# Optimization experiments

Measured on AMD Instinct MI355X. Metric: run time of the kernel, lower is better.

## Reference

```python
import jax, jax.numpy as jnp
import numpy as np

# BCQLinear packed forward: weight[o, i] reconstructed from per-(out,group,bit)
# alpha scales and +/-1 binary codes via einsum('oib,oiab->oia'), then a plain
# out-channel-wise matmul (in_ch_wise=False) plus bias. beta is NOT used in the
# packed forward path of the original module.

B, S = 2, 1024          # token dims (m...)
O = 4096                 # out_features
G, A, NB = 32, 128, 3    # n_groups, group_size, n_bits; in_features = G*A = 4096


def setup_inputs() -> dict:
    key = jax.random.key(0)
    k1, k2, k3, k4 = jax.random.split(key, 4)
    x = jax.random.normal(k1, (B, S, G * A), dtype=jnp.float32)
    # binary codes are strictly +/-1 (Packer.unpack yields sign bits)
    b = jnp.sign(jax.random.normal(k2, (O, G, A, NB)))
    binary = jnp.where(b == 0, 1.0, b).astype(jnp.float32)
    # alpha scales are small positive magnitudes in practice
    alpha = jax.random.uniform(k3, (O, G, NB), dtype=jnp.float32,
                               minval=0.01, maxval=0.1)
    bias = 0.01 * jax.random.normal(k4, (O,), dtype=jnp.float32)
    return {"input": x, "binary": binary, "alpha": alpha, "bias": bias}


def reference(input, binary, alpha, bias):
    # dequantize: [O, G, A] -> [O, I]
    weight = jnp.einsum('oib,oiab->oia', alpha, binary).reshape(binary.shape[0], -1)
    # out-channel-wise matmul: m...i, oi -> m...o
    out = jnp.einsum('msi,oi->mso', input, weight) + bias
    return out
```

## Files before the change

### kernel.cpp

```cpp
#include <hip/hip_runtime.h>
#include <hip/hip_bf16.h>
#include <stdint.h>

typedef __bf16 bf16x8 __attribute__((ext_vector_type(8)));
typedef __bf16 bf16x4 __attribute__((ext_vector_type(4)));
typedef float  f32x4  __attribute__((ext_vector_type(4)));

static constexpr int Mdim = 2048;
static constexpr int Ndim = 4096;
static constexpr int Kdim = 4096;
static constexpr int DQ_BLOCKS = (Ndim * Kdim / 4) / 256;
static constexpr int CVT_BLOCKS = (Mdim * Kdim / 8) / 256;

__global__ __launch_bounds__(256)
void prep(const float* __restrict__ binary, const float* __restrict__ alpha,
          const float* __restrict__ x, __bf16* __restrict__ w,
          __bf16* __restrict__ xb) {
  const int b = blockIdx.x;
  if (b < DQ_BLOCKS) {
    long e = ((long)b * 256 + threadIdx.x) * 4;
    int o = (int)(e >> 12);
    int i = (int)(e & 4095);
    int g = i >> 7;
    const float* al = alpha + ((long)o * 32 + g) * 3;
    float a0 = al[0], a1 = al[1], a2 = al[2];
    const float4* bs = (const float4*)(binary + e * 3);
    float4 b0 = bs[0], b1 = bs[1], b2 = bs[2];
    bf16x4 wv;
    wv[0] = (__bf16)(a0 * b0.x + a1 * b0.y + a2 * b0.z);
    wv[1] = (__bf16)(a0 * b0.w + a1 * b1.x + a2 * b1.y);
    wv[2] = (__bf16)(a0 * b1.z + a1 * b1.w + a2 * b2.x);
    wv[3] = (__bf16)(a0 * b2.y + a1 * b2.z + a2 * b2.w);
    *(bf16x4*)(w + e) = wv;
  } else {
    long e = ((long)(b - DQ_BLOCKS) * 256 + threadIdx.x) * 8;
    float4 v0 = *(const float4*)(x + e);
    float4 v1 = *(const float4*)(x + e + 4);
    bf16x8 r;
    r[0] = (__bf16)v0.x; r[1] = (__bf16)v0.y; r[2] = (__bf16)v0.z; r[3] = (__bf16)v0.w;
    r[4] = (__bf16)v1.x; r[5] = (__bf16)v1.y; r[6] = (__bf16)v1.z; r[7] = (__bf16)v1.w;
    *(bf16x8*)(xb + e) = r;
  }
}

static constexpr int NT = Kdim / 64;
static constexpr int BUF = 49152;

__device__ __forceinline__ void g2l16(const void* g, void* l) {
  __builtin_amdgcn_global_load_lds(
      (const __attribute__((address_space(1))) void*)g,
      (__attribute__((address_space(3))) void*)l, 16, 0, 0);
}

#define BAR()    __builtin_amdgcn_s_barrier()
#define LGKM0()  asm volatile("s_waitcnt lgkmcnt(0)" ::: "memory")
#define SCHED0() __builtin_amdgcn_sched_barrier(0)
#define VMC6()   asm volatile("s_waitcnt vmcnt(6)" ::: "memory")
#define VMC0()   asm volatile("s_waitcnt vmcnt(0)" ::: "memory")

#define STAGE_A(t, H, bo) do { \
  _Pragma("unroll") for (int j_ = 0; j_ < 2; ++j_) \
    g2l16(baseA[j_] + (H) * 128 * (long)Kdim + (t) * 64, \
          sm + (bo) + (H) * 16384 + (w * 2 + j_) * 1024); \
} while (0)
#define STAGE_B(t, bo) do { \
  _Pragma("unroll") for (int j_ = 0; j_ < 2; ++j_) \
    g2l16(baseB[j_] + (t) * 64, \
          sm + (bo) + 32768 + (w * 2 + j_) * 1024); \
} while (0)

#define LOAD_A4(dst, bo, m0_) do { \
  _Pragma("unroll") for (int m_ = 0; m_ < 4; ++m_) \
    _Pragma("unroll") for (int h_ = 0; h_ < 2; ++h_) \
      dst[m_][h_] = *(const bf16x8*)(sm + (bo) + aoffbase + ((m0_) + m_) * 2048 + swz[h_]); \
} while (0)
#define LOAD_B2(dst, bo) do { \
  _Pragma("unroll") for (int n_ = 0; n_ < 2; ++n_) \
    _Pragma("unroll") for (int h_ = 0; h_ < 2; ++h_) \
      dst[n_][h_] = *(const bf16x8*)(sm + (bo) + boffbase + n_ * 2048 + swz[h_]); \
} while (0)

#define MMA16(fa_, fb_, m0_) do { \
  __builtin_amdgcn_s_setprio(1); \
  _Pragma("unroll") for (int m_ = 0; m_ < 4; ++m_) \
    _Pragma("unroll") for (int n_ = 0; n_ < 2; ++n_) { \
      acc[(m0_) + m_][n_] = __builtin_amdgcn_mfma_f32_16x16x32_bf16( \
          fa_[m_][0], fb_[n_][0], acc[(m0_) + m_][n_], 0, 0, 0); \
      acc[(m0_) + m_][n_] = __builtin_amdgcn_mfma_f32_16x16x32_bf16( \
          fa_[m_][1], fb_[n_][1], acc[(m0_) + m_][n_], 0, 0, 0); \
    } \
  __builtin_amdgcn_s_setprio(0); \
} while (0)

__global__ __launch_bounds__(512, 2)
void gemm3(const __bf16* __restrict__ A, const __bf16* __restrict__ Bw,
           const float* __restrict__ bias, float* __restrict__ out) {
  __shared__ __align__(128) char sm[3 * BUF];
  const int tid = threadIdx.x, lane = tid & 63, w = tid >> 6;
  const int wm = w >> 2, wn = w & 3;

  const int bid = blockIdx.x;
  const int logical = (bid & 7) * 32 + (bid >> 3);
  const int tm = logical & 7;
  const int tn = logical >> 3;

  const int rlo = lane >> 3;
  const int gsw = (lane & 7) ^ rlo;
  const __bf16* baseA[2];
  const __bf16* baseB[2];
#pragma unroll
  for (int j = 0; j < 2; ++j) {
    int rp = (w * 2 + j) * 8 + rlo;
    baseA[j] = A  + (long)(tm * 256 + rp) * Kdim + gsw * 8;
    baseB[j] = Bw + (long)(tn * 128 + rp) * Kdim + gsw * 8;
  }

  int swz[2];
#pragma unroll
  for (int h = 0; h < 2; ++h)
    swz[h] = (((h * 4 + (lane >> 4)) ^ (lane & 7)) << 4);
  const int aoffbase = (wm * 128 + (lane & 15)) * 128;
  const int boffbase = 32768 + (wn * 32 + (lane & 15)) * 128;

  f32x4 acc[8][2] = {};

  STAGE_A(0, 0, 0);     STAGE_A(0, 1, 0);     STAGE_B(0, 0);
  STAGE_A(1, 0, BUF);   STAGE_A(1, 1, BUF);   STAGE_B(1, BUF);
  VMC6();
  BAR();

  bf16x8 fa[4][2], fa2[4][2], fb[2][2];
  int ba = 0, bb = BUF, bc = 2 * BUF;

  for (int t = 0; t < NT; ++t) {
    const bool pf = (t + 2 < NT);
    LOAD_A4(fa, ba, 0);
    LOAD_B2(fb, ba);
    if (pf) STAGE_A(t + 2, 0, bc);
    BAR(); LGKM0(); SCHED0();
    MMA16(fa, fb, 0);
    BAR();
    LOAD_A4(fa2, ba, 4);
    if (pf) { STAGE_A(t + 2, 1, bc); STAGE_B(t + 2, bc); }
    if (t < NT - 2) { VMC6(); } else { VMC0(); }
    BAR(); LGKM0(); SCHED0();
    MMA16(fa2, fb, 4);
    BAR();
    int tmp = ba; ba = bb; bb = bc; bc = tmp;
  }

  const int r4 = (lane >> 4) * 4;
  const int cl = lane & 15;
#pragma unroll
  for (int n = 0; n < 2; ++n) {
    const int col = tn * 128 + wn * 32 + n * 16 + cl;
    const float bv = bias[col];
#pragma unroll
    for (int m = 0; m < 8; ++m)
#pragma unroll
      for (int r = 0; r < 4; ++r) {
        const int row = tm * 256 + wm * 128 + m * 16 + r4 + r;
        out[(long)row * Ndim + col] = acc[m][n][r] + bv;
      }
  }
}

extern "C" void kernel_launch(void* const* d_in, const int* in_sizes, int n_in,
                              void* d_out, int out_size, void* d_ws, size_t ws_size,
                              hipStream_t stream) {
  const float* x      = (const float*)d_in[0];
  const float* binary = (const float*)d_in[1];
  const float* alpha  = (const float*)d_in[2];
  const float* bias   = (const float*)d_in[3];
  float* out = (float*)d_out;

  __bf16* wb = (__bf16*)d_ws;
  __bf16* xb = wb + (size_t)Ndim * Kdim;

  prep<<<dim3(DQ_BLOCKS + CVT_BLOCKS), 256, 0, stream>>>(binary, alpha, x, wb, xb);
  gemm3<<<dim3(256), 512, 0, stream>>>(xb, wb, bias, out);
}
```

Measured before the change: 122.8 us.

## Transpose GEMM tile to 128x256, stage epilogue through LDS, widen dequant

```diff
diff --git a/kernel.cpp b/kernel.cpp
--- a/kernel.cpp
+++ b/kernel.cpp
@@ -3,13 +3,12 @@
 #include <stdint.h>
 
 typedef __bf16 bf16x8 __attribute__((ext_vector_type(8)));
-typedef __bf16 bf16x4 __attribute__((ext_vector_type(4)));
 typedef float  f32x4  __attribute__((ext_vector_type(4)));
 
 static constexpr int Mdim = 2048;
 static constexpr int Ndim = 4096;
 static constexpr int Kdim = 4096;
-static constexpr int DQ_BLOCKS = (Ndim * Kdim / 4) / 256;
+static constexpr int DQ_BLOCKS = (Ndim * Kdim / 8) / 256;
 static constexpr int CVT_BLOCKS = (Mdim * Kdim / 8) / 256;
 
 __global__ __launch_bounds__(256)
@@ -18,20 +17,23 @@
           __bf16* __restrict__ xb) {
   const int b = blockIdx.x;
   if (b < DQ_BLOCKS) {
-    long e = ((long)b * 256 + threadIdx.x) * 4;
+    long e = ((long)b * 256 + threadIdx.x) * 8;
     int o = (int)(e >> 12);
-    int i = (int)(e & 4095);
-    int g = i >> 7;
+    int g = (int)((e & 4095) >> 7);
     const float* al = alpha + ((long)o * 32 + g) * 3;
     float a0 = al[0], a1 = al[1], a2 = al[2];
-    const float4* bs = (const float4*)(binary + e * 3);
-    float4 b0 = bs[0], b1 = bs[1], b2 = bs[2];
-    bf16x4 wv;
-    wv[0] = (__bf16)(a0 * b0.x + a1 * b0.y + a2 * b0.z);
-    wv[1] = (__bf16)(a0 * b0.w + a1 * b1.x + a2 * b1.y);
-    wv[2] = (__bf16)(a0 * b1.z + a1 * b1.w + a2 * b2.x);
-    wv[3] = (__bf16)(a0 * b2.y + a1 * b2.z + a2 * b2.w);
-    *(bf16x4*)(w + e) = wv;
+    const float4* q = (const float4*)(binary + e * 3);
+    float4 q0 = q[0], q1 = q[1], q2 = q[2], q3 = q[3], q4 = q[4], q5 = q[5];
+    bf16x8 wv;
+    wv[0] = (__bf16)(a0 * q0.x + a1 * q0.y + a2 * q0.z);
+    wv[1] = (__bf16)(a0 * q0.w + a1 * q1.x + a2 * q1.y);
+    wv[2] = (__bf16)(a0 * q1.z + a1 * q1.w + a2 * q2.x);
+    wv[3] = (__bf16)(a0 * q2.y + a1 * q2.z + a2 * q2.w);
+    wv[4] = (__bf16)(a0 * q3.x + a1 * q3.y + a2 * q3.z);
+    wv[5] = (__bf16)(a0 * q3.w + a1 * q4.x + a2 * q4.y);
+    wv[6] = (__bf16)(a0 * q4.z + a1 * q4.w + a2 * q5.x);
+    wv[7] = (__bf16)(a0 * q5.y + a1 * q5.z + a2 * q5.w);
+    *(bf16x8*)(w + e) = wv;
   } else {
     long e = ((long)(b - DQ_BLOCKS) * 256 + threadIdx.x) * 8;
     float4 v0 = *(const float4*)(x + e);
@@ -58,42 +60,40 @@
 #define VMC6()   asm volatile("s_waitcnt vmcnt(6)" ::: "memory")
 #define VMC0()   asm volatile("s_waitcnt vmcnt(0)" ::: "memory")
 
-#define STAGE_A(t, H, bo) do { \
+#define STAGE_A(t, bo) do { \
   _Pragma("unroll") for (int j_ = 0; j_ < 2; ++j_) \
-    g2l16(baseA[j_] + (H) * 128 * (long)Kdim + (t) * 64, \
-          sm + (bo) + (H) * 16384 + (w * 2 + j_) * 1024); \
+    g2l16(baseA[j_] + (t) * 64, sm + (bo) + (w * 2 + j_) * 1024); \
 } while (0)
 #define STAGE_B(t, bo) do { \
-  _Pragma("unroll") for (int j_ = 0; j_ < 2; ++j_) \
-    g2l16(baseB[j_] + (t) * 64, \
-          sm + (bo) + 32768 + (w * 2 + j_) * 1024); \
+  _Pragma("unroll") for (int j_ = 0; j_ < 4; ++j_) \
+    g2l16(baseB[j_] + (t) * 64, sm + (bo) + 16384 + (w * 4 + j_) * 1024); \
 } while (0)
 
-#define LOAD_A4(dst, bo, m0_) do { \
+#define LOAD_A4(dst, bo) do { \
   _Pragma("unroll") for (int m_ = 0; m_ < 4; ++m_) \
     _Pragma("unroll") for (int h_ = 0; h_ < 2; ++h_) \
-      dst[m_][h_] = *(const bf16x8*)(sm + (bo) + aoffbase + ((m0_) + m_) * 2048 + swz[h_]); \
+      dst[m_][h_] = *(const bf16x8*)(sm + (bo) + aoffbase + m_ * 2048 + swz[h_]); \
 } while (0)
-#define LOAD_B2(dst, bo) do { \
+#define LOAD_B2(dst, bo, n0_) do { \
   _Pragma("unroll") for (int n_ = 0; n_ < 2; ++n_) \
     _Pragma("unroll") for (int h_ = 0; h_ < 2; ++h_) \
-      dst[n_][h_] = *(const bf16x8*)(sm + (bo) + boffbase + n_ * 2048 + swz[h_]); \
+      dst[n_][h_] = *(const bf16x8*)(sm + (bo) + boffbase + ((n0_) + n_) * 2048 + swz[h_]); \
 } while (0)
 
-#define MMA16(fa_, fb_, m0_) do { \
+#define MMA16(fa_, fb_, n0_) do { \
   __builtin_amdgcn_s_setprio(1); \
   _Pragma("unroll") for (int m_ = 0; m_ < 4; ++m_) \
     _Pragma("unroll") for (int n_ = 0; n_ < 2; ++n_) { \
-      acc[(m0_) + m_][n_] = __builtin_amdgcn_mfma_f32_16x16x32_bf16( \
-          fa_[m_][0], fb_[n_][0], acc[(m0_) + m_][n_], 0, 0, 0); \
-      acc[(m0_) + m_][n_] = __builtin_amdgcn_mfma_f32_16x16x32_bf16( \
-          fa_[m_][1], fb_[n_][1], acc[(m0_) + m_][n_], 0, 0, 0); \
+      acc[m_][(n0_) + n_] = __builtin_amdgcn_mfma_f32_16x16x32_bf16( \
+          fa_[m_][0], fb_[n_][0], acc[m_][(n0_) + n_], 0, 0, 0); \
+      acc[m_][(n0_) + n_] = __builtin_amdgcn_mfma_f32_16x16x32_bf16( \
+          fa_[m_][1], fb_[n_][1], acc[m_][(n0_) + n_], 0, 0, 0); \
     } \
   __builtin_amdgcn_s_setprio(0); \
 } while (0)
 
 __global__ __launch_bounds__(512, 2)
-void gemm3(const __bf16* __restrict__ A, const __bf16* __restrict__ Bw,
+void gemm4(const __bf16* __restrict__ A, const __bf16* __restrict__ Bw,
            const float* __restrict__ bias, float* __restrict__ out) {
   __shared__ __align__(128) char sm[3 * BUF];
   const int tid = threadIdx.x, lane = tid & 63, w = tid >> 6;
@@ -101,67 +101,77 @@
 
   const int bid = blockIdx.x;
   const int logical = (bid & 7) * 32 + (bid >> 3);
-  const int tm = logical & 7;
-  const int tn = logical >> 3;
+  const int tm = logical & 15;
+  const int tn = logical >> 4;
 
   const int rlo = lane >> 3;
   const int gsw = (lane & 7) ^ rlo;
   const __bf16* baseA[2];
-  const __bf16* baseB[2];
+  const __bf16* baseB[4];
 #pragma unroll
-  for (int j = 0; j < 2; ++j) {
-    int rp = (w * 2 + j) * 8 + rlo;
-    baseA[j] = A  + (long)(tm * 256 + rp) * Kdim + gsw * 8;
-    baseB[j] = Bw + (long)(tn * 128 + rp) * Kdim + gsw * 8;
-  }
+  for (int j = 0; j < 2; ++j)
+    baseA[j] = A + (long)(tm * 128 + w * 16 + j * 8 + rlo) * Kdim + gsw * 8;
+#pragma unroll
+  for (int j = 0; j < 4; ++j)
+    baseB[j] = Bw + (long)(tn * 256 + w * 32 + j * 8 + rlo) * Kdim + gsw * 8;
 
   int swz[2];
 #pragma unroll
   for (int h = 0; h < 2; ++h)
     swz[h] = (((h * 4 + (lane >> 4)) ^ (lane & 7)) << 4);
-  const int aoffbase = (wm * 128 + (lane & 15)) * 128;
-  const int boffbase = 32768 + (wn * 32 + (lane & 15)) * 128;
+  const int aoffbase = (wm * 64 + (lane & 15)) * 128;
+  const int boffbase = 16384 + (wn * 64 + (lane & 15)) * 128;
 
-  f32x4 acc[8][2] = {};
+  f32x4 acc[4][4] = {};
 
-  STAGE_A(0, 0, 0);     STAGE_A(0, 1, 0);     STAGE_B(0, 0);
-  STAGE_A(1, 0, BUF);   STAGE_A(1, 1, BUF);   STAGE_B(1, BUF);
+  STAGE_A(0, 0);   STAGE_B(0, 0);
+  STAGE_A(1, BUF); STAGE_B(1, BUF);
   VMC6();
   BAR();
 
-  bf16x8 fa[4][2], fa2[4][2], fb[2][2];
+  bf16x8 fa[4][2], fb01[2][2], fb23[2][2];
   int ba = 0, bb = BUF, bc = 2 * BUF;
 
   for (int t = 0; t < NT; ++t) {
     const bool pf = (t + 2 < NT);
-    LOAD_A4(fa, ba, 0);
-    LOAD_B2(fb, ba);
-    if (pf) STAGE_A(t + 2, 0, bc);
+    LOAD_A4(fa, ba);
+    LOAD_B2(fb01, ba, 0);
+    if (pf) STAGE_A(t + 2, bc);
     BAR(); LGKM0(); SCHED0();
-    MMA16(fa, fb, 0);
+    MMA16(fa, fb01, 0);
     BAR();
-    LOAD_A4(fa2, ba, 4);
-    if (pf) { STAGE_A(t + 2, 1, bc); STAGE_B(t + 2, bc); }
+    LOAD_B2(fb23, ba, 2);
+    if (pf) STAGE_B(t + 2, bc);
     if (t < NT - 2) { VMC6(); } else { VMC0(); }
     BAR(); LGKM0(); SCHED0();
-    MMA16(fa2, fb, 4);
+    MMA16(fa, fb23, 2);
     BAR();
     int tmp = ba; ba = bb; bb = bc; bc = tmp;
   }
 
+  float* lf = (float*)sm;
   const int r4 = (lane >> 4) * 4;
   const int cl = lane & 15;
 #pragma unroll
-  for (int n = 0; n < 2; ++n) {
-    const int col = tn * 128 + wn * 32 + n * 16 + cl;
-    const float bv = bias[col];
+  for (int m = 0; m < 4; ++m)
 #pragma unroll
-    for (int m = 0; m < 8; ++m)
+    for (int n = 0; n < 4; ++n)
 #pragma unroll
       for (int r = 0; r < 4; ++r) {
-        const int row = tm * 256 + wm * 128 + m * 16 + r4 + r;
-        out[(long)row * Ndim + col] = acc[m][n][r] + bv;
+        int row = wm * 64 + m * 16 + r4 + r;
+        int col = wn * 64 + n * 16 + cl;
+        lf[row * 260 + col] = acc[m][n][r];
       }
+  __syncthreads();
+#pragma unroll
+  for (int i = 0; i < 16; ++i) {
+    int idx = tid + i * 512;
+    int row = idx >> 6;
+    int c4 = idx & 63;
+    f32x4 v = *(const f32x4*)(lf + row * 260 + c4 * 4);
+    float4 bv = *(const float4*)(bias + tn * 256 + c4 * 4);
+    v[0] += bv.x; v[1] += bv.y; v[2] += bv.z; v[3] += bv.w;
+    *(f32x4*)(out + (long)(tm * 128 + row) * Ndim + tn * 256 + c4 * 4) = v;
   }
 }
 
@@ -178,5 +188,5 @@
   __bf16* xb = wb + (size_t)Ndim * Kdim;
 
   prep<<<dim3(DQ_BLOCKS + CVT_BLOCKS), 256, 0, stream>>>(binary, alpha, x, wb, xb);
-  gemm3<<<dim3(256), 512, 0, stream>>>(xb, wb, bias, out);
+  gemm4<<<dim3(256), 512, 0, stream>>>(xb, wb, bias, out);
 }
```

Result: no change. 120.7 us (-1.7%).
